# Kernel tuning notes

Hardware: AMD Instinct MI355X
Metric: run time of the kernel (lower is better)

Reference implementation:

```python
import math
import jax, jax.numpy as jnp
import numpy as np

D, H, FF, V, L, B, S = 512, 8, 2048, 10000, 6, 8, 512
DK = D // H
EPS = 1e-5


def posenc(seq_len, d_model):
    pos = np.arange(seq_len, dtype=np.float32)[:, None]
    div = np.exp(np.arange(0, d_model, 2, dtype=np.float32) * (-math.log(10000.0) / d_model))
    pe = np.zeros((seq_len, d_model), dtype=np.float32)
    pe[:, 0::2] = np.sin(pos * div)
    pe[:, 1::2] = np.cos(pos * div)
    return jnp.asarray(pe)


def layernorm(x, g, b):
    mu = jnp.mean(x, axis=-1, keepdims=True)
    var = jnp.mean(jnp.square(x - mu), axis=-1, keepdims=True)
    return (x - mu) * jax.lax.rsqrt(var + EPS) * g + b


def mha(x_q, x_kv, w, b, mask):
    # w: [4, D, D] (q,k,v,o), b: [4, D]; mask broadcastable to [B,H,Sq,Sk] (bool)
    Bq, Sq, _ = x_q.shape
    Sk = x_kv.shape[1]
    q = (x_q @ w[0] + b[0]).reshape(Bq, Sq, H, DK).transpose(0, 2, 1, 3)
    k = (x_kv @ w[1] + b[1]).reshape(Bq, Sk, H, DK).transpose(0, 2, 1, 3)
    v = (x_kv @ w[2] + b[2]).reshape(Bq, Sk, H, DK).transpose(0, 2, 1, 3)
    scores = jnp.einsum('bhqd,bhkd->bhqk', q, k) / jnp.sqrt(jnp.float32(DK))
    if mask is not None:
        scores = jnp.where(mask, scores, -jnp.inf)
    attn = jax.nn.softmax(scores, axis=-1)
    out = jnp.einsum('bhqk,bhkd->bhqd', attn, v)
    out = out.transpose(0, 2, 1, 3).reshape(Bq, Sq, D)
    return out @ w[3] + b[3]


def ffn(x, w1, b1, w2, b2):
    return jax.nn.relu(x @ w1 + b1) @ w2 + b2


def setup_inputs() -> dict:
    key = jax.random.key(0)
    ks = iter(jax.random.split(key, 32))
    std = 0.02
    n = lambda shape: jax.random.normal(next(ks), shape, dtype=jnp.float32) * std
    inp = {
        'src': jax.random.randint(next(ks), (B, S), 0, V),
        'tgt': jax.random.randint(next(ks), (B, S), 0, V),
        'src_emb': n((V, D)),
        'tgt_emb': n((V, D)),
        'enc_qkvo_w': n((L, 4, D, D)), 'enc_qkvo_b': jnp.zeros((L, 4, D)),
        'enc_ff1_w': n((L, D, FF)), 'enc_ff1_b': jnp.zeros((L, FF)),
        'enc_ff2_w': n((L, FF, D)), 'enc_ff2_b': jnp.zeros((L, D)),
        'enc_ln_g': jnp.ones((L, 2, D)), 'enc_ln_b': jnp.zeros((L, 2, D)),
        'dec_sa_w': n((L, 4, D, D)), 'dec_sa_b': jnp.zeros((L, 4, D)),
        'dec_ca_w': n((L, 4, D, D)), 'dec_ca_b': jnp.zeros((L, 4, D)),
        'dec_ff1_w': n((L, D, FF)), 'dec_ff1_b': jnp.zeros((L, FF)),
        'dec_ff2_w': n((L, FF, D)), 'dec_ff2_b': jnp.zeros((L, D)),
        'dec_ln_g': jnp.ones((L, 3, D)), 'dec_ln_b': jnp.zeros((L, 3, D)),
        'out_w': n((D, V)), 'out_b': jnp.zeros((V,)),
    }
    return inp


def reference(src, tgt, src_emb, tgt_emb,
              enc_qkvo_w, enc_qkvo_b, enc_ff1_w, enc_ff1_b, enc_ff2_w, enc_ff2_b,
              enc_ln_g, enc_ln_b,
              dec_sa_w, dec_sa_b, dec_ca_w, dec_ca_b,
              dec_ff1_w, dec_ff1_b, dec_ff2_w, dec_ff2_b, dec_ln_g, dec_ln_b,
              out_w, out_b):
    pe = posenc(S, D)
    # masks (derived from tokens, pad_token=0), as in the driver
    src_pad = (src != 0)[:, None, None, :]                 # [B,1,1,S]
    tgt_pad = (tgt != 0)[:, None, None, :]                 # [B,1,1,S]
    look_ahead = jnp.tril(jnp.ones((S, S), bool))[None, None]  # [1,1,S,S]

    # encoder (dropout is identity in eval)
    x = src_emb[src] + pe[None]
    for l in range(L):
        a = mha(x, x, enc_qkvo_w[l], enc_qkvo_b[l], src_pad)
        x = layernorm(x + a, enc_ln_g[l, 0], enc_ln_b[l, 0])
        f = ffn(x, enc_ff1_w[l], enc_ff1_b[l], enc_ff2_w[l], enc_ff2_b[l])
        x = layernorm(x + f, enc_ln_g[l, 1], enc_ln_b[l, 1])
    enc_out = x

    # decoder
    y = tgt_emb[tgt] + pe[None]
    for l in range(L):
        a = mha(y, y, dec_sa_w[l], dec_sa_b[l], look_ahead)
        y = layernorm(y + a, dec_ln_g[l, 0], dec_ln_b[l, 0])
        c = mha(y, enc_out, dec_ca_w[l], dec_ca_b[l], tgt_pad)
        y = layernorm(y + c, dec_ln_g[l, 1], dec_ln_b[l, 1])
        f = ffn(y, dec_ff1_w[l], dec_ff1_b[l], dec_ff2_w[l], dec_ff2_b[l])
        y = layernorm(y + f, dec_ln_g[l, 2], dec_ln_b[l, 2])

    return y @ out_w + out_b  # [B, S, V]
```

## Files before the change

### kernel.cpp

```cpp
#include <hip/hip_runtime.h>
#include <hip/hip_bf16.h>
#include <math.h>

#define D 512
#define H 8
#define FF 2048
#define V 10000
#define NLAYERS 6
#define BB 8
#define S 512
#define DK 64
#define BS (BB*S)

typedef float WT;
typedef float OT;

__device__ __forceinline__ float tof(float x){ return x; }

__global__ __launch_bounds__(256) void embed_kernel(const int* __restrict__ tok,
                                                    const WT* __restrict__ emb,
                                                    float* __restrict__ x)
{
    int r = blockIdx.x;
    int s = r % S;
    int tk = tok[r];
    int t = threadIdx.x;
    const float c = -logf(10000.f) / (float)D;
#pragma unroll
    for (int p = 0; p < 2; ++p) {
        int d = t + p * 256;
        int i2 = d & ~1;
        float ang = (float)s * expf((float)i2 * c);
        float pe = (d & 1) ? cosf(ang) : sinf(ang);
        x[(long)r * D + d] = tof(emb[(long)tk * D + d]) + pe;
    }
}

__global__ __launch_bounds__(256) void softmax_kernel(float* __restrict__ sc,
                                                      const int* __restrict__ tok,
                                                      int causal)
{
    __shared__ float red[4];
    long r = blockIdx.x;
    int i = (int)(r % S);
    int b = (int)(r / ((long)H * S));
    float* row = sc + r * (long)S;
    int t = threadIdx.x;
    float v0 = row[t], v1 = row[t + 256];
    if (causal) {
        if (t > i)        v0 = -INFINITY;
        if (t + 256 > i)  v1 = -INFINITY;
    } else {
        if (tok[b * S + t] == 0)        v0 = -INFINITY;
        if (tok[b * S + t + 256] == 0)  v1 = -INFINITY;
    }
    float m = fmaxf(v0, v1);
    for (int off = 32; off; off >>= 1) m = fmaxf(m, __shfl_down(m, off));
    if ((t & 63) == 0) red[t >> 6] = m;
    __syncthreads();
    m = fmaxf(fmaxf(red[0], red[1]), fmaxf(red[2], red[3]));
    __syncthreads();
    float e0 = expf(v0 - m), e1 = expf(v1 - m);
    float ssum = e0 + e1;
    for (int off = 32; off; off >>= 1) ssum += __shfl_down(ssum, off);
    if ((t & 63) == 0) red[t >> 6] = ssum;
    __syncthreads();
    ssum = red[0] + red[1] + red[2] + red[3];
    float inv = 1.0f / ssum;
    row[t]       = e0 * inv;
    row[t + 256] = e1 * inv;
}

__global__ __launch_bounds__(256) void ln_kernel(float* __restrict__ x,
                                                 const float* __restrict__ a,
                                                 const WT* __restrict__ g,
                                                 const WT* __restrict__ bb)
{
    __shared__ float red[4];
    long r = blockIdx.x;
    float* xr = x + r * D;
    const float* ar = a + r * D;
    int t = threadIdx.x;
    float v0 = xr[t] + ar[t];
    float v1 = xr[t + 256] + ar[t + 256];
    float s = v0 + v1;
    for (int off = 32; off; off >>= 1) s += __shfl_down(s, off);
    if ((t & 63) == 0) red[t >> 6] = s;
    __syncthreads();
    float mu = (red[0] + red[1] + red[2] + red[3]) * (1.0f / D);
    __syncthreads();
    float d0 = v0 - mu, d1 = v1 - mu;
    float q = d0 * d0 + d1 * d1;
    for (int off = 32; off; off >>= 1) q += __shfl_down(q, off);
    if ((t & 63) == 0) red[t >> 6] = q;
    __syncthreads();
    float var = (red[0] + red[1] + red[2] + red[3]) * (1.0f / D);
    float inv = rsqrtf(var + 1e-5f);
    xr[t]       = d0 * inv * tof(g[t])       + tof(bb[t]);
    xr[t + 256] = d1 * inv * tof(g[t + 256]) + tof(bb[t + 256]);
}

typedef __attribute__((ext_vector_type(8))) short bf16x8;
typedef __attribute__((ext_vector_type(4))) float f32x4;

__device__ __forceinline__ void splitf(float x, short& h, short& l)
{
    unsigned u = __float_as_uint(x);
    h = (short)(u >> 16);
    float hf = __uint_as_float(u & 0xffff0000u);
    unsigned v = __float_as_uint(x - hf);
    l = (short)((v + 0x7fffu + ((v >> 16) & 1u)) >> 16);
}

template<int BM, int BN, bool TRANSB, bool RELU>
__global__ __launch_bounds__(256, 2) void mm_kernel(
    const float* __restrict__ A, int lda, long sAb, long sAh,
    const float* __restrict__ Bm, int ldb, long sBb, long sBh,
    const float* __restrict__ bias, long sbias,
    float* __restrict__ C, int ldc, long sCb, long sCh,
    int M, int N, int K, int Hdiv, float alpha)
{
    constexpr int MREP = BM / 32;
    constexpr int NREP = BN / 32;
    __shared__ __align__(16) char ldsA[BM * 128];
    __shared__ __align__(16) char ldsB[BN * 128];

    int z = blockIdx.z;
    int zb = z / Hdiv, zh = z % Hdiv;
    A  += (long)zb * sAb + (long)zh * sAh;
    Bm += (long)zb * sBb + (long)zh * sBh;
    C  += (long)zb * sCb + (long)zh * sCh;
    const float* bp = bias ? (bias + (long)zh * sbias) : nullptr;

    int m0 = blockIdx.y * BM;
    int n0 = blockIdx.x * BN;
    int t  = threadIdx.x;
    int g  = t & 3;
    int rr = t >> 2;
    int l  = t & 63;
    int w  = t >> 6;
    int wm = w >> 1, wn = w & 1;
    int lr = l & 15, kg = l >> 4;

    int aoh[MREP], aol[MREP], boh[NREP], bol[NREP];
#pragma unroll
    for (int mi = 0; mi < MREP; ++mi) {
        int r = wm * (BM / 2) + mi * 16 + lr;
        aoh[mi] = r * 128 + (((2 * kg)     ^ (r & 7)) << 4);
        aol[mi] = r * 128 + (((2 * kg + 1) ^ (r & 7)) << 4);
    }
#pragma unroll
    for (int ni = 0; ni < NREP; ++ni) {
        int r = wn * (BN / 2) + ni * 16 + lr;
        boh[ni] = r * 128 + (((2 * kg)     ^ (r & 7)) << 4);
        bol[ni] = r * 128 + (((2 * kg + 1) ^ (r & 7)) << 4);
    }

    f32x4 acc[MREP][NREP];
#pragma unroll
    for (int mi = 0; mi < MREP; ++mi)
#pragma unroll
        for (int ni = 0; ni < NREP; ++ni)
            acc[mi][ni] = (f32x4){0.f, 0.f, 0.f, 0.f};

    for (int k0 = 0; k0 < K; k0 += 32) {
        if (k0) __syncthreads();
#pragma unroll
        for (int i = 0; i < BM / 64; ++i) {
            int r = rr + 64 * i;
            const float4* p = (const float4*)(A + (long)(m0 + r) * lda + (k0 + 8 * g));
            float4 f0 = p[0], f1 = p[1];
            float f[8] = {f0.x, f0.y, f0.z, f0.w, f1.x, f1.y, f1.z, f1.w};
            bf16x8 hv, lv;
#pragma unroll
            for (int j = 0; j < 8; ++j) { short hh, ll; splitf(f[j], hh, ll); hv[j] = hh; lv[j] = ll; }
            char* rd = ldsA + r * 128;
            *(bf16x8*)(rd + (((2 * g)     ^ (r & 7)) << 4)) = hv;
            *(bf16x8*)(rd + (((2 * g + 1) ^ (r & 7)) << 4)) = lv;
        }
#pragma unroll
        for (int i = 0; i < BN / 64; ++i) {
            int r = rr + 64 * i;
            float f[8];
            if (TRANSB) {
                const float4* p = (const float4*)(Bm + (long)(n0 + r) * ldb + (k0 + 8 * g));
                float4 f0 = p[0], f1 = p[1];
                f[0]=f0.x; f[1]=f0.y; f[2]=f0.z; f[3]=f0.w;
                f[4]=f1.x; f[5]=f1.y; f[6]=f1.z; f[7]=f1.w;
            } else {
                int gn = n0 + r;
                bool ok = gn < N;
                const float* p = Bm + (long)(k0 + 8 * g) * ldb + gn;
#pragma unroll
                for (int j = 0; j < 8; ++j) f[j] = ok ? p[(long)j * ldb] : 0.f;
            }
            bf16x8 hv, lv;
#pragma unroll
            for (int j = 0; j < 8; ++j) { short hh, ll; splitf(f[j], hh, ll); hv[j] = hh; lv[j] = ll; }
            char* rd = ldsB + r * 128;
            *(bf16x8*)(rd + (((2 * g)     ^ (r & 7)) << 4)) = hv;
            *(bf16x8*)(rd + (((2 * g + 1) ^ (r & 7)) << 4)) = lv;
        }
        __syncthreads();
        bf16x8 ah[MREP], al_[MREP], bh[NREP], bl_[NREP];
#pragma unroll
        for (int mi = 0; mi < MREP; ++mi) {
            ah[mi]  = *(const bf16x8*)(ldsA + aoh[mi]);
            al_[mi] = *(const bf16x8*)(ldsA + aol[mi]);
        }
#pragma unroll
        for (int ni = 0; ni < NREP; ++ni) {
            bh[ni]  = *(const bf16x8*)(ldsB + boh[ni]);
            bl_[ni] = *(const bf16x8*)(ldsB + bol[ni]);
        }
#pragma unroll
        for (int mi = 0; mi < MREP; ++mi)
#pragma unroll
            for (int ni = 0; ni < NREP; ++ni) {
                acc[mi][ni] = __builtin_amdgcn_mfma_f32_16x16x32_bf16(ah[mi],  bh[ni],  acc[mi][ni], 0, 0, 0);
                acc[mi][ni] = __builtin_amdgcn_mfma_f32_16x16x32_bf16(ah[mi],  bl_[ni], acc[mi][ni], 0, 0, 0);
                acc[mi][ni] = __builtin_amdgcn_mfma_f32_16x16x32_bf16(al_[mi], bh[ni],  acc[mi][ni], 0, 0, 0);
            }
    }
#pragma unroll
    for (int mi = 0; mi < MREP; ++mi) {
        int mrow = m0 + wm * (BM / 2) + mi * 16 + kg * 4;
#pragma unroll
        for (int ni = 0; ni < NREP; ++ni) {
            int col = n0 + wn * (BN / 2) + ni * 16 + lr;
            if (col < N) {
                float bv = bp ? bp[col] : 0.f;
#pragma unroll
                for (int j = 0; j < 4; ++j) {
                    float v2 = acc[mi][ni][j] * alpha + bv;
                    if (RELU) v2 = fmaxf(v2, 0.f);
                    C[(long)(mrow + j) * ldc + col] = v2;
                }
            }
        }
    }
}

extern "C" void kernel_launch(void* const* d_in, const int* in_sizes, int n_in,
                              void* d_out, int out_size, void* d_ws, size_t ws_size,
                              hipStream_t stream)
{
    const int* src      = (const int*)d_in[0];
    const int* tgt      = (const int*)d_in[1];
    const WT*  src_emb  = (const WT*)d_in[2];
    const WT*  tgt_emb  = (const WT*)d_in[3];
    const WT* enc_qkvo_w = (const WT*)d_in[4];
    const WT* enc_qkvo_b = (const WT*)d_in[5];
    const WT* enc_ff1_w  = (const WT*)d_in[6];
    const WT* enc_ff1_b  = (const WT*)d_in[7];
    const WT* enc_ff2_w  = (const WT*)d_in[8];
    const WT* enc_ff2_b  = (const WT*)d_in[9];
    const WT* enc_ln_g   = (const WT*)d_in[10];
    const WT* enc_ln_b   = (const WT*)d_in[11];
    const WT* dec_sa_w   = (const WT*)d_in[12];
    const WT* dec_sa_b   = (const WT*)d_in[13];
    const WT* dec_ca_w   = (const WT*)d_in[14];
    const WT* dec_ca_b   = (const WT*)d_in[15];
    const WT* dec_ff1_w  = (const WT*)d_in[16];
    const WT* dec_ff1_b  = (const WT*)d_in[17];
    const WT* dec_ff2_w  = (const WT*)d_in[18];
    const WT* dec_ff2_b  = (const WT*)d_in[19];
    const WT* dec_ln_g   = (const WT*)d_in[20];
    const WT* dec_ln_b   = (const WT*)d_in[21];
    const WT* out_w      = (const WT*)d_in[22];
    const WT* out_b      = (const WT*)d_in[23];
    OT* out = (OT*)d_out;

    float* bx   = (float*)d_ws;
    float* by   = bx   + (size_t)BS * D;
    float* bmha = by   + (size_t)BS * D;
    float* bq   = bmha + (size_t)BS * D;
    float* bk   = bq   + (size_t)BS * D;
    float* bv   = bk   + (size_t)BS * D;
    float* batt = bq;
    float* bsc  = bv   + (size_t)BS * D;
    float* bffn = bsc;

    dim3 blk(256);

    auto attn = [&](const float* xq, const float* xkv, const WT* w, const WT* b,
                    const int* masktok, int causal, float* outbuf) {
        if (xq == xkv) {
            dim3 g(D / 128, BS / 128, 3);
            mm_kernel<128, 128, false, false><<<g, blk, 0, stream>>>(
                xq, D, 0, 0, w, D, 0, (long)D * D, b, D,
                bq, D, 0, (long)BS * D, BS, D, D, 3, 1.0f);
        } else {
            dim3 gq(D / 64, BS / 128, 1);
            mm_kernel<128, 64, false, false><<<gq, blk, 0, stream>>>(
                xq, D, 0, 0, w, D, 0, 0, b, 0,
                bq, D, 0, 0, BS, D, D, 1, 1.0f);
            dim3 gkv(D / 128, BS / 128, 2);
            mm_kernel<128, 128, false, false><<<gkv, blk, 0, stream>>>(
                xkv, D, 0, 0, w + (size_t)D * D, D, 0, (long)D * D, b + D, D,
                bk, D, 0, (long)BS * D, BS, D, D, 2, 1.0f);
        }
        {
            dim3 g(S / 128, S / 128, BB * H);
            mm_kernel<128, 128, true, false><<<g, blk, 0, stream>>>(
                bq, D, (long)S * D, DK, bk, D, (long)S * D, DK, nullptr, 0,
                bsc, S, (long)H * S * S, (long)S * S, S, S, DK, H, 0.125f);
        }
        softmax_kernel<<<dim3(BB * H * S), blk, 0, stream>>>(bsc, masktok, causal);
        {
            dim3 g(1, S / 64, BB * H);
            mm_kernel<64, 64, false, false><<<g, blk, 0, stream>>>(
                bsc, S, (long)H * S * S, (long)S * S, bv, D, (long)S * D, DK, nullptr, 0,
                batt, D, (long)S * D, DK, S, DK, S, H, 1.0f);
        }
        {
            dim3 g(D / 64, BS / 128, 1);
            mm_kernel<128, 64, false, false><<<g, blk, 0, stream>>>(
                batt, D, 0, 0, w + 3 * (size_t)D * D, D, 0, 0, b + 3 * D, 0,
                outbuf, D, 0, 0, BS, D, D, 1, 1.0f);
        }
    };

    auto ffn = [&](float* x, const WT* w1, const WT* b1, const WT* w2, const WT* b2) {
        dim3 g1(FF / 128, BS / 128, 1);
        mm_kernel<128, 128, false, true><<<g1, blk, 0, stream>>>(
            x, D, 0, 0, w1, FF, 0, 0, b1, 0,
            bffn, FF, 0, 0, BS, FF, D, 1, 1.0f);
        dim3 g2(D / 64, BS / 128, 1);
        mm_kernel<128, 64, false, false><<<g2, blk, 0, stream>>>(
            bffn, FF, 0, 0, w2, D, 0, 0, b2, 0,
            bmha, D, 0, 0, BS, D, FF, 1, 1.0f);
    };

    embed_kernel<<<dim3(BS), blk, 0, stream>>>(src, src_emb, bx);
    for (int l = 0; l < NLAYERS; ++l) {
        const WT* w = enc_qkvo_w + (size_t)l * 4 * D * D;
        const WT* b = enc_qkvo_b + (size_t)l * 4 * D;
        attn(bx, bx, w, b, src, 0, bmha);
        ln_kernel<<<dim3(BS), blk, 0, stream>>>(bx, bmha,
            enc_ln_g + (size_t)l * 2 * D, enc_ln_b + (size_t)l * 2 * D);
        ffn(bx, enc_ff1_w + (size_t)l * D * FF, enc_ff1_b + (size_t)l * FF,
            enc_ff2_w + (size_t)l * FF * D, enc_ff2_b + (size_t)l * D);
        ln_kernel<<<dim3(BS), blk, 0, stream>>>(bx, bmha,
            enc_ln_g + (size_t)l * 2 * D + D, enc_ln_b + (size_t)l * 2 * D + D);
    }

    embed_kernel<<<dim3(BS), blk, 0, stream>>>(tgt, tgt_emb, by);
    for (int l = 0; l < NLAYERS; ++l) {
        attn(by, by, dec_sa_w + (size_t)l * 4 * D * D, dec_sa_b + (size_t)l * 4 * D,
             nullptr, 1, bmha);
        ln_kernel<<<dim3(BS), blk, 0, stream>>>(by, bmha,
            dec_ln_g + (size_t)l * 3 * D, dec_ln_b + (size_t)l * 3 * D);
        attn(by, bx, dec_ca_w + (size_t)l * 4 * D * D, dec_ca_b + (size_t)l * 4 * D,
             tgt, 0, bmha);
        ln_kernel<<<dim3(BS), blk, 0, stream>>>(by, bmha,
            dec_ln_g + (size_t)l * 3 * D + D, dec_ln_b + (size_t)l * 3 * D + D);
        ffn(by, dec_ff1_w + (size_t)l * D * FF, dec_ff1_b + (size_t)l * FF,
            dec_ff2_w + (size_t)l * FF * D, dec_ff2_b + (size_t)l * D);
        ln_kernel<<<dim3(BS), blk, 0, stream>>>(by, bmha,
            dec_ln_g + (size_t)l * 3 * D + 2 * D, dec_ln_b + (size_t)l * 3 * D + 2 * D);
    }

    {
        dim3 g((V + 127) / 128, BS / 128, 1);
        mm_kernel<128, 128, false, false><<<g, blk, 0, stream>>>(
            by, D, 0, 0, out_w, V, 0, 0, out_b, 0,
            out, V, 0, 0, BS, V, D, 1, 1.0f);
    }
}
```

Measured before the change: 6.200 ms.

## Pre-split activations and weights into packed bf16 hi/lo words for GEMMs

Producers (embed, layernorm, GEMM epilogues) now also write a packed hi/lo bf16 split of each fp32 value. Weights are split and transposed into K-contiguous layout each call by a new wsplit kernel, so GEMM tile loads become coalesced 16-byte loads with only bit shuffles instead of per-element splitting and strided B gathers. Attention scores are processed in two halves of heads to reduce score buffer footprint. The cost is extra writes, additional weight-split kernels per layer, and more launches.

```diff
diff --git a/kernel.cpp b/kernel.cpp
--- a/kernel.cpp
+++ b/kernel.cpp
@@ -1,5 +1,4 @@
 #include <hip/hip_runtime.h>
-#include <hip/hip_bf16.h>
 #include <math.h>
 
 #define D 512
@@ -15,11 +14,29 @@
 typedef float WT;
 typedef float OT;
 
-__device__ __forceinline__ float tof(float x){ return x; }
+__device__ __forceinline__ unsigned packsplit(float v)
+{
+    unsigned u = __float_as_uint(v);
+    unsigned h = u & 0xffff0000u;
+    float r = v - __uint_as_float(h);
+    unsigned w = __float_as_uint(r);
+    unsigned l = (w + 0x7fffu + ((w >> 16) & 1u)) >> 16;
+    return h | (l & 0xffffu);
+}
+
+__device__ __forceinline__ void splitf(float x, unsigned short& h, unsigned short& l)
+{
+    unsigned u = __float_as_uint(x);
+    h = (unsigned short)(u >> 16);
+    float hf = __uint_as_float(u & 0xffff0000u);
+    unsigned v = __float_as_uint(x - hf);
+    l = (unsigned short)((v + 0x7fffu + ((v >> 16) & 1u)) >> 16);
+}
 
 __global__ __launch_bounds__(256) void embed_kernel(const int* __restrict__ tok,
                                                     const WT* __restrict__ emb,
-                                                    float* __restrict__ x)
+                                                    float* __restrict__ x,
+                                                    unsigned* __restrict__ xs)
 {
     int r = blockIdx.x;
     int s = r % S;
@@ -32,18 +49,20 @@
         int i2 = d & ~1;
         float ang = (float)s * expf((float)i2 * c);
         float pe = (d & 1) ? cosf(ang) : sinf(ang);
-        x[(long)r * D + d] = tof(emb[(long)tk * D + d]) + pe;
+        float v = emb[(long)tk * D + d] + pe;
+        x[(long)r * D + d] = v;
+        xs[(long)r * D + d] = packsplit(v);
     }
 }
 
 __global__ __launch_bounds__(256) void softmax_kernel(float* __restrict__ sc,
                                                       const int* __restrict__ tok,
-                                                      int causal)
+                                                      int causal, int rbase)
 {
     __shared__ float red[4];
     long r = blockIdx.x;
     int i = (int)(r % S);
-    int b = (int)(r / ((long)H * S));
+    int b = (int)(((long)rbase + r) / ((long)H * S));
     float* row = sc + r * (long)S;
     int t = threadIdx.x;
     float v0 = row[t], v1 = row[t + 256];
@@ -74,7 +93,8 @@
 __global__ __launch_bounds__(256) void ln_kernel(float* __restrict__ x,
                                                  const float* __restrict__ a,
                                                  const WT* __restrict__ g,
-                                                 const WT* __restrict__ bb)
+                                                 const WT* __restrict__ bb,
+                                                 unsigned* __restrict__ xs)
 {
     __shared__ float red[4];
     long r = blockIdx.x;
@@ -96,28 +116,60 @@
     __syncthreads();
     float var = (red[0] + red[1] + red[2] + red[3]) * (1.0f / D);
     float inv = rsqrtf(var + 1e-5f);
-    xr[t]       = d0 * inv * tof(g[t])       + tof(bb[t]);
-    xr[t + 256] = d1 * inv * tof(g[t + 256]) + tof(bb[t + 256]);
-}
+    float o0 = d0 * inv * g[t]       + bb[t];
+    float o1 = d1 * inv * g[t + 256] + bb[t + 256];
+    xr[t]       = o0;
+    xr[t + 256] = o1;
+    xs[r * D + t]       = packsplit(o0);
+    xs[r * D + t + 256] = packsplit(o1);
+}
+
+__global__ __launch_bounds__(256) void wsplit_kernel(const float* __restrict__ W,
+                                                     unsigned* __restrict__ O,
+                                                     int K, int N)
+{
+    __shared__ unsigned tb[64][65];
+    long zoff = (long)blockIdx.z * K * N;
+    W += zoff; O += zoff;
+    int n0 = blockIdx.x * 64, k0 = blockIdx.y * 64;
+    int t = threadIdx.x;
+#pragma unroll
+    for (int i = 0; i < 16; ++i) {
+        int idx = t + 256 * i;
+        int kk = idx >> 6, nn = idx & 63;
+        int gn = n0 + nn;
+        float v = (gn < N) ? W[(long)(k0 + kk) * N + gn] : 0.f;
+        tb[nn][kk] = packsplit(v);
+    }
+    __syncthreads();
+#pragma unroll
+    for (int i = 0; i < 4; ++i) {
+        int idx = t + 256 * i;
+        int nn = idx >> 4, kk = (idx & 15) * 4;
+        int gn = n0 + nn;
+        if (gn < N) {
+            uint4 o;
+            o.x = tb[nn][kk]; o.y = tb[nn][kk + 1];
+            o.z = tb[nn][kk + 2]; o.w = tb[nn][kk + 3];
+            *(uint4*)&O[(long)gn * K + k0 + kk] = o;
+        }
+    }
+}
+
+#define A_SPLIT 0
+#define A_F32   1
+#define B_SPLIT 0
+#define B_GATH  1
 
 typedef __attribute__((ext_vector_type(8))) short bf16x8;
 typedef __attribute__((ext_vector_type(4))) float f32x4;
 
-__device__ __forceinline__ void splitf(float x, short& h, short& l)
-{
-    unsigned u = __float_as_uint(x);
-    h = (short)(u >> 16);
-    float hf = __uint_as_float(u & 0xffff0000u);
-    unsigned v = __float_as_uint(x - hf);
-    l = (short)((v + 0x7fffu + ((v >> 16) & 1u)) >> 16);
-}
-
-template<int BM, int BN, bool TRANSB, bool RELU>
+template<int BM, int BN, int AMODE, int BMODE, bool RELU, bool CSPLIT>
 __global__ __launch_bounds__(256, 2) void mm_kernel(
-    const float* __restrict__ A, int lda, long sAb, long sAh,
-    const float* __restrict__ Bm, int ldb, long sBb, long sBh,
+    const void* __restrict__ Av, int lda, long sAb, long sAh,
+    const void* __restrict__ Bv, int ldb, long sBb, long sBh,
     const float* __restrict__ bias, long sbias,
-    float* __restrict__ C, int ldc, long sCb, long sCh,
+    void* __restrict__ Cv, int ldc, long sCb, long sCh,
     int M, int N, int K, int Hdiv, float alpha)
 {
     constexpr int MREP = BM / 32;
@@ -126,10 +178,10 @@
     __shared__ __align__(16) char ldsB[BN * 128];
 
     int z = blockIdx.z;
-    int zb = z / Hdiv, zh = z % Hdiv;
-    A  += (long)zb * sAb + (long)zh * sAh;
-    Bm += (long)zb * sBb + (long)zh * sBh;
-    C  += (long)zb * sCb + (long)zh * sCh;
+    int zb = z / Hdiv, zh = z - zb * Hdiv;
+    long aoff = (long)zb * sAb + (long)zh * sAh;
+    long boff = (long)zb * sBb + (long)zh * sBh;
+    long coff = (long)zb * sCb + (long)zh * sCh;
     const float* bp = bias ? (bias + (long)zh * sbias) : nullptr;
 
     int m0 = blockIdx.y * BM;
@@ -165,41 +217,100 @@
 
     for (int k0 = 0; k0 < K; k0 += 32) {
         if (k0) __syncthreads();
-#pragma unroll
-        for (int i = 0; i < BM / 64; ++i) {
-            int r = rr + 64 * i;
-            const float4* p = (const float4*)(A + (long)(m0 + r) * lda + (k0 + 8 * g));
-            float4 f0 = p[0], f1 = p[1];
-            float f[8] = {f0.x, f0.y, f0.z, f0.w, f1.x, f1.y, f1.z, f1.w};
-            bf16x8 hv, lv;
-#pragma unroll
-            for (int j = 0; j < 8; ++j) { short hh, ll; splitf(f[j], hh, ll); hv[j] = hh; lv[j] = ll; }
-            char* rd = ldsA + r * 128;
-            *(bf16x8*)(rd + (((2 * g)     ^ (r & 7)) << 4)) = hv;
-            *(bf16x8*)(rd + (((2 * g + 1) ^ (r & 7)) << 4)) = lv;
-        }
-#pragma unroll
-        for (int i = 0; i < BN / 64; ++i) {
-            int r = rr + 64 * i;
-            float f[8];
-            if (TRANSB) {
-                const float4* p = (const float4*)(Bm + (long)(n0 + r) * ldb + (k0 + 8 * g));
+        if (AMODE == A_SPLIT) {
+            const unsigned* A = (const unsigned*)Av + aoff;
+#pragma unroll
+            for (int i = 0; i < BM / 64; ++i) {
+                int r = rr + 64 * i;
+                const uint4* p = (const uint4*)(A + (long)(m0 + r) * lda + (k0 + 8 * g));
+                uint4 q0 = p[0], q1 = p[1];
+                uint4 hv, lv;
+                hv.x = (q0.x >> 16) | (q0.y & 0xffff0000u);
+                hv.y = (q0.z >> 16) | (q0.w & 0xffff0000u);
+                hv.z = (q1.x >> 16) | (q1.y & 0xffff0000u);
+                hv.w = (q1.z >> 16) | (q1.w & 0xffff0000u);
+                lv.x = (q0.x & 0xffffu) | (q0.y << 16);
+                lv.y = (q0.z & 0xffffu) | (q0.w << 16);
+                lv.z = (q1.x & 0xffffu) | (q1.y << 16);
+                lv.w = (q1.z & 0xffffu) | (q1.w << 16);
+                char* rd = ldsA + r * 128;
+                *(uint4*)(rd + (((2 * g)     ^ (r & 7)) << 4)) = hv;
+                *(uint4*)(rd + (((2 * g + 1) ^ (r & 7)) << 4)) = lv;
+            }
+        } else {
+            const float* A = (const float*)Av + aoff;
+#pragma unroll
+            for (int i = 0; i < BM / 64; ++i) {
+                int r = rr + 64 * i;
+                const float4* p = (const float4*)(A + (long)(m0 + r) * lda + (k0 + 8 * g));
                 float4 f0 = p[0], f1 = p[1];
-                f[0]=f0.x; f[1]=f0.y; f[2]=f0.z; f[3]=f0.w;
-                f[4]=f1.x; f[5]=f1.y; f[6]=f1.z; f[7]=f1.w;
-            } else {
+                float f[8] = {f0.x, f0.y, f0.z, f0.w, f1.x, f1.y, f1.z, f1.w};
+                uint4 hv, lv;
+                unsigned hw[4], lw[4];
+#pragma unroll
+                for (int jj = 0; jj < 4; ++jj) {
+                    unsigned short h0, l0, h1, l1;
+                    splitf(f[2 * jj], h0, l0);
+                    splitf(f[2 * jj + 1], h1, l1);
+                    hw[jj] = (unsigned)h0 | ((unsigned)h1 << 16);
+                    lw[jj] = (unsigned)l0 | ((unsigned)l1 << 16);
+                }
+                hv.x = hw[0]; hv.y = hw[1]; hv.z = hw[2]; hv.w = hw[3];
+                lv.x = lw[0]; lv.y = lw[1]; lv.z = lw[2]; lv.w = lw[3];
+                char* rd = ldsA + r * 128;
+                *(uint4*)(rd + (((2 * g)     ^ (r & 7)) << 4)) = hv;
+                *(uint4*)(rd + (((2 * g + 1) ^ (r & 7)) << 4)) = lv;
+            }
+        }
+        if (BMODE == B_SPLIT) {
+            const unsigned* B = (const unsigned*)Bv + boff;
+#pragma unroll
+            for (int i = 0; i < BN / 64; ++i) {
+                int r = rr + 64 * i;
                 int gn = n0 + r;
-                bool ok = gn < N;
-                const float* p = Bm + (long)(k0 + 8 * g) * ldb + gn;
-#pragma unroll
-                for (int j = 0; j < 8; ++j) f[j] = ok ? p[(long)j * ldb] : 0.f;
-            }
-            bf16x8 hv, lv;
-#pragma unroll
-            for (int j = 0; j < 8; ++j) { short hh, ll; splitf(f[j], hh, ll); hv[j] = hh; lv[j] = ll; }
-            char* rd = ldsB + r * 128;
-            *(bf16x8*)(rd + (((2 * g)     ^ (r & 7)) << 4)) = hv;
-            *(bf16x8*)(rd + (((2 * g + 1) ^ (r & 7)) << 4)) = lv;
+                uint4 hv, lv;
+                if (gn < N) {
+                    const uint4* p = (const uint4*)(B + (long)gn * ldb + (k0 + 8 * g));
+                    uint4 q0 = p[0], q1 = p[1];
+                    hv.x = (q0.x >> 16) | (q0.y & 0xffff0000u);
+                    hv.y = (q0.z >> 16) | (q0.w & 0xffff0000u);
+                    hv.z = (q1.x >> 16) | (q1.y & 0xffff0000u);
+                    hv.w = (q1.z >> 16) | (q1.w & 0xffff0000u);
+                    lv.x = (q0.x & 0xffffu) | (q0.y << 16);
+                    lv.y = (q0.z & 0xffffu) | (q0.w << 16);
+                    lv.z = (q1.x & 0xffffu) | (q1.y << 16);
+                    lv.w = (q1.z & 0xffffu) | (q1.w << 16);
+                } else {
+                    hv.x = hv.y = hv.z = hv.w = 0u;
+                    lv.x = lv.y = lv.z = lv.w = 0u;
+                }
+                char* rd = ldsB + r * 128;
+                *(uint4*)(rd + (((2 * g)     ^ (r & 7)) << 4)) = hv;
+                *(uint4*)(rd + (((2 * g + 1) ^ (r & 7)) << 4)) = lv;
+            }
+        } else {
+            const unsigned* B = (const unsigned*)Bv + boff;
+#pragma unroll
+            for (int i = 0; i < BN / 64; ++i) {
+                int r = rr + 64 * i;
+                int gn = n0 + r;
+                unsigned e[8];
+                const unsigned* p = B + (long)(k0 + 8 * g) * ldb + gn;
+#pragma unroll
+                for (int j = 0; j < 8; ++j) e[j] = (gn < N) ? p[(long)j * ldb] : 0u;
+                uint4 hv, lv;
+                hv.x = (e[0] >> 16) | (e[1] & 0xffff0000u);
+                hv.y = (e[2] >> 16) | (e[3] & 0xffff0000u);
+                hv.z = (e[4] >> 16) | (e[5] & 0xffff0000u);
+                hv.w = (e[6] >> 16) | (e[7] & 0xffff0000u);
+                lv.x = (e[0] & 0xffffu) | (e[1] << 16);
+                lv.y = (e[2] & 0xffffu) | (e[3] << 16);
+                lv.z = (e[4] & 0xffffu) | (e[5] << 16);
+                lv.w = (e[6] & 0xffffu) | (e[7] << 16);
+                char* rd = ldsB + r * 128;
+                *(uint4*)(rd + (((2 * g)     ^ (r & 7)) << 4)) = hv;
+                *(uint4*)(rd + (((2 * g + 1) ^ (r & 7)) << 4)) = lv;
+            }
         }
         __syncthreads();
         bf16x8 ah[MREP], al_[MREP], bh[NREP], bl_[NREP];
@@ -229,12 +340,14 @@
         for (int ni = 0; ni < NREP; ++ni) {
             int col = n0 + wn * (BN / 2) + ni * 16 + lr;
             if (col < N) {
-                float bv = bp ? bp[col] : 0.f;
+                float bvl = bp ? bp[col] : 0.f;
 #pragma unroll
                 for (int j = 0; j < 4; ++j) {
-                    float v2 = acc[mi][ni][j] * alpha + bv;
+                    float v2 = acc[mi][ni][j] * alpha + bvl;
                     if (RELU) v2 = fmaxf(v2, 0.f);
-                    C[(long)(mrow + j) * ldc + col] = v2;
+                    long ci = coff + (long)(mrow + j) * ldc + col;
+                    if (CSPLIT) ((unsigned*)Cv)[ci] = packsplit(v2);
+                    else        ((float*)Cv)[ci] = v2;
                 }
             }
         }
@@ -271,100 +384,109 @@
     const WT* out_b      = (const WT*)d_in[23];
     OT* out = (OT*)d_out;
 
-    float* bx   = (float*)d_ws;
-    float* by   = bx   + (size_t)BS * D;
-    float* bmha = by   + (size_t)BS * D;
-    float* bq   = bmha + (size_t)BS * D;
-    float* bk   = bq   + (size_t)BS * D;
-    float* bv   = bk   + (size_t)BS * D;
-    float* batt = bq;
-    float* bsc  = bv   + (size_t)BS * D;
-    float* bffn = bsc;
+    const size_t NE = (size_t)BS * D;
+    float*    bx   = (float*)d_ws;
+    float*    by   = bx + NE;
+    float*    bmha = by + NE;
+    unsigned* bxs  = (unsigned*)(bmha + NE);
+    unsigned* bys  = bxs + NE;
+    unsigned* bqs  = bys + NE;
+    unsigned* bks  = bqs + NE;
+    unsigned* bvs  = bks + NE;
+    unsigned* wsp  = bvs + NE;
+    float*    bsc  = (float*)(wsp + (size_t)D * FF);
+    unsigned* hidden = (unsigned*)bsc;
+    unsigned* batts  = bqs;
+    unsigned* vws    = bqs;
 
     dim3 blk(256);
 
-    auto attn = [&](const float* xq, const float* xkv, const WT* w, const WT* b,
+    auto attn = [&](const unsigned* aqs, const unsigned* akvs,
+                    const WT* w, const WT* b,
                     const int* masktok, int causal, float* outbuf) {
-        if (xq == xkv) {
-            dim3 g(D / 128, BS / 128, 3);
-            mm_kernel<128, 128, false, false><<<g, blk, 0, stream>>>(
-                xq, D, 0, 0, w, D, 0, (long)D * D, b, D,
-                bq, D, 0, (long)BS * D, BS, D, D, 3, 1.0f);
+        wsplit_kernel<<<dim3(8, 8, 4), blk, 0, stream>>>(w, wsp, D, D);
+        if (aqs == akvs) {
+            mm_kernel<128, 128, A_SPLIT, B_SPLIT, false, true>
+                <<<dim3(4, 32, 3), blk, 0, stream>>>(
+                aqs, D, 0, 0, wsp, D, 0, (long)D * D, b, D,
+                bqs, D, 0, (long)BS * D, BS, D, D, 3, 1.0f);
         } else {
-            dim3 gq(D / 64, BS / 128, 1);
-            mm_kernel<128, 64, false, false><<<gq, blk, 0, stream>>>(
-                xq, D, 0, 0, w, D, 0, 0, b, 0,
-                bq, D, 0, 0, BS, D, D, 1, 1.0f);
-            dim3 gkv(D / 128, BS / 128, 2);
-            mm_kernel<128, 128, false, false><<<gkv, blk, 0, stream>>>(
-                xkv, D, 0, 0, w + (size_t)D * D, D, 0, (long)D * D, b + D, D,
-                bk, D, 0, (long)BS * D, BS, D, D, 2, 1.0f);
-        }
-        {
-            dim3 g(S / 128, S / 128, BB * H);
-            mm_kernel<128, 128, true, false><<<g, blk, 0, stream>>>(
-                bq, D, (long)S * D, DK, bk, D, (long)S * D, DK, nullptr, 0,
+            mm_kernel<128, 64, A_SPLIT, B_SPLIT, false, true>
+                <<<dim3(8, 32, 1), blk, 0, stream>>>(
+                aqs, D, 0, 0, wsp, D, 0, 0, b, 0,
+                bqs, D, 0, 0, BS, D, D, 1, 1.0f);
+            mm_kernel<128, 128, A_SPLIT, B_SPLIT, false, true>
+                <<<dim3(4, 32, 2), blk, 0, stream>>>(
+                akvs, D, 0, 0, wsp + (size_t)D * D, D, 0, (long)D * D, b + D, D,
+                bks, D, 0, (long)BS * D, BS, D, D, 2, 1.0f);
+        }
+        for (int hh = 0; hh < 2; ++hh) {
+            long zo = (long)hh * 4 * S * D;
+            mm_kernel<128, 128, A_SPLIT, B_SPLIT, false, false>
+                <<<dim3(4, 4, 32), blk, 0, stream>>>(
+                bqs + zo, D, (long)S * D, DK, bks + zo, D, (long)S * D, DK,
+                nullptr, 0,
                 bsc, S, (long)H * S * S, (long)S * S, S, S, DK, H, 0.125f);
-        }
-        softmax_kernel<<<dim3(BB * H * S), blk, 0, stream>>>(bsc, masktok, causal);
-        {
-            dim3 g(1, S / 64, BB * H);
-            mm_kernel<64, 64, false, false><<<g, blk, 0, stream>>>(
-                bsc, S, (long)H * S * S, (long)S * S, bv, D, (long)S * D, DK, nullptr, 0,
-                batt, D, (long)S * D, DK, S, DK, S, H, 1.0f);
-        }
-        {
-            dim3 g(D / 64, BS / 128, 1);
-            mm_kernel<128, 64, false, false><<<g, blk, 0, stream>>>(
-                batt, D, 0, 0, w + 3 * (size_t)D * D, D, 0, 0, b + 3 * D, 0,
-                outbuf, D, 0, 0, BS, D, D, 1, 1.0f);
-        }
+            softmax_kernel<<<dim3(BB * H * S / 2), blk, 0, stream>>>(
+                bsc, masktok, causal, hh * (BB * H * S / 2));
+            mm_kernel<64, 64, A_F32, B_GATH, false, true>
+                <<<dim3(1, 8, 32), blk, 0, stream>>>(
+                bsc, S, (long)H * S * S, (long)S * S, bvs + zo, D, (long)S * D, DK,
+                nullptr, 0,
+                batts + zo, D, (long)S * D, DK, S, DK, S, H, 1.0f);
+        }
+        mm_kernel<128, 64, A_SPLIT, B_SPLIT, false, false>
+            <<<dim3(8, 32, 1), blk, 0, stream>>>(
+            batts, D, 0, 0, wsp + (size_t)3 * D * D, D, 0, 0, b + 3 * D, 0,
+            outbuf, D, 0, 0, BS, D, D, 1, 1.0f);
     };
 
-    auto ffn = [&](float* x, const WT* w1, const WT* b1, const WT* w2, const WT* b2) {
-        dim3 g1(FF / 128, BS / 128, 1);
-        mm_kernel<128, 128, false, true><<<g1, blk, 0, stream>>>(
-            x, D, 0, 0, w1, FF, 0, 0, b1, 0,
-            bffn, FF, 0, 0, BS, FF, D, 1, 1.0f);
-        dim3 g2(D / 64, BS / 128, 1);
-        mm_kernel<128, 64, false, false><<<g2, blk, 0, stream>>>(
-            bffn, FF, 0, 0, w2, D, 0, 0, b2, 0,
+    auto ffn = [&](const unsigned* xs, const WT* w1, const WT* b1,
+                   const WT* w2, const WT* b2) {
+        wsplit_kernel<<<dim3(FF / 64, D / 64, 1), blk, 0, stream>>>(w1, wsp, D, FF);
+        mm_kernel<128, 128, A_SPLIT, B_SPLIT, true, true>
+            <<<dim3(FF / 128, BS / 128, 1), blk, 0, stream>>>(
+            xs, D, 0, 0, wsp, D, 0, 0, b1, 0,
+            hidden, FF, 0, 0, BS, FF, D, 1, 1.0f);
+        wsplit_kernel<<<dim3(D / 64, FF / 64, 1), blk, 0, stream>>>(w2, wsp, FF, D);
+        mm_kernel<128, 64, A_SPLIT, B_SPLIT, false, false>
+            <<<dim3(8, 32, 1), blk, 0, stream>>>(
+            hidden, FF, 0, 0, wsp, FF, 0, 0, b2, 0,
             bmha, D, 0, 0, BS, D, FF, 1, 1.0f);
     };
 
-    embed_kernel<<<dim3(BS), blk, 0, stream>>>(src, src_emb, bx);
+    embed_kernel<<<dim3(BS), blk, 0, stream>>>(src, src_emb, bx, bxs);
     for (int l = 0; l < NLAYERS; ++l) {
-        const WT* w = enc_qkvo_w + (size_t)l * 4 * D * D;
-        const WT* b = enc_qkvo_b + (size_t)l * 4 * D;
-        attn(bx, bx, w, b, src, 0, bmha);
+        attn(bxs, bxs, enc_qkvo_w + (size_t)l * 4 * D * D,
+             enc_qkvo_b + (size_t)l * 4 * D, src, 0, bmha);
         ln_kernel<<<dim3(BS), blk, 0, stream>>>(bx, bmha,
-            enc_ln_g + (size_t)l * 2 * D, enc_ln_b + (size_t)l * 2 * D);
-        ffn(bx, enc_ff1_w + (size_t)l * D * FF, enc_ff1_b + (size_t)l * FF,
+            enc_ln_g + (size_t)l * 2 * D, enc_ln_b + (size_t)l * 2 * D, bxs);
+        ffn(bxs, enc_ff1_w + (size_t)l * D * FF, enc_ff1_b + (size_t)l * FF,
             enc_ff2_w + (size_t)l * FF * D, enc_ff2_b + (size_t)l * D);
         ln_kernel<<<dim3(BS), blk, 0, stream>>>(bx, bmha,
-            enc_ln_g + (size_t)l * 2 * D + D, enc_ln_b + (size_t)l * 2 * D + D);
-    }
-
-    embed_kernel<<<dim3(BS), blk, 0, stream>>>(tgt, tgt_emb, by);
+            enc_ln_g + (size_t)l * 2 * D + D, enc_ln_b + (size_t)l * 2 * D + D, bxs);
+    }
+
+    embed_kernel<<<dim3(BS), blk, 0, stream>>>(tgt, tgt_emb, by, bys);
     for (int l = 0; l < NLAYERS; ++l) {
-        attn(by, by, dec_sa_w + (size_t)l * 4 * D * D, dec_sa_b + (size_t)l * 4 * D,
-             nullptr, 1, bmha);
+        attn(bys, bys, dec_sa_w + (size_t)l * 4 * D * D,
+             dec_sa_b + (size_t)l * 4 * D, nullptr, 1, bmha);
         ln_kernel<<<dim3(BS), blk, 0, stream>>>(by, bmha,
-            dec_ln_g + (size_t)l * 3 * D, dec_ln_b + (size_t)l * 3 * D);
-        attn(by, bx, dec_ca_w + (size_t)l * 4 * D * D, dec_ca_b + (size_t)l * 4 * D,
-             tgt, 0, bmha);
+            dec_ln_g + (size_t)l * 3 * D, dec_ln_b + (size_t)l * 3 * D, bys);
+        attn(bys, bxs, dec_ca_w + (size_t)l * 4 * D * D,
+             dec_ca_b + (size_t)l * 4 * D, tgt, 0, bmha);
         ln_kernel<<<dim3(BS), blk, 0, stream>>>(by, bmha,
-            dec_ln_g + (size_t)l * 3 * D + D, dec_ln_b + (size_t)l * 3 * D + D);
-        ffn(by, dec_ff1_w + (size_t)l * D * FF, dec_ff1_b + (size_t)l * FF,
+            dec_ln_g + (size_t)l * 3 * D + D, dec_ln_b + (size_t)l * 3 * D + D, bys);
+        ffn(bys, dec_ff1_w + (size_t)l * D * FF, dec_ff1_b + (size_t)l * FF,
             dec_ff2_w + (size_t)l * FF * D, dec_ff2_b + (size_t)l * D);
         ln_kernel<<<dim3(BS), blk, 0, stream>>>(by, bmha,
-            dec_ln_g + (size_t)l * 3 * D + 2 * D, dec_ln_b + (size_t)l * 3 * D + 2 * D);
-    }
-
-    {
-        dim3 g((V + 127) / 128, BS / 128, 1);
-        mm_kernel<128, 128, false, false><<<g, blk, 0, stream>>>(
-            by, D, 0, 0, out_w, V, 0, 0, out_b, 0,
-            out, V, 0, 0, BS, V, D, 1, 1.0f);
-    }
-}
+            dec_ln_g + (size_t)l * 3 * D + 2 * D, dec_ln_b + (size_t)l * 3 * D + 2 * D,
+            bys);
+    }
+
+    wsplit_kernel<<<dim3((V + 63) / 64, D / 64, 1), blk, 0, stream>>>(out_w, vws, D, V);
+    mm_kernel<128, 128, A_SPLIT, B_SPLIT, false, false>
+        <<<dim3((V + 127) / 128, BS / 128, 1), blk, 0, stream>>>(
+        bys, D, 0, 0, vws, D, 0, 0, out_b, 0,
+        out, V, 0, 0, BS, V, D, 1, 1.0f);
+}
```

After: 5.889 ms. -5.0%, faster.
